# Optimization experiments

Measured on AMD Instinct MI355X. Metric: run time of the kernel, lower is better.

Reference implementation:

```python
import jax, jax.numpy as jnp
import numpy as np

N, T, D, H = 32, 512, 1024, 1024

def setup_inputs() -> dict:
    key = jax.random.key(0)
    k1, k2, k3, k4 = jax.random.split(key, 4)
    x = jax.random.normal(k1, (N, T, D), dtype=jnp.float32)
    prev_ht = jax.random.normal(k2, (N, H), dtype=jnp.float32)
    # scale like a fan-in init so sigmoid/tanh stay in sane range
    weight = jax.random.normal(k3, (D + H, 3 * (D + H)), dtype=jnp.float32) / np.sqrt(D + H)
    bias = jax.random.normal(k4, (3 * (D + H),), dtype=jnp.float32) * 0.01
    return {"x": x, "prev_ht": prev_ht, "weight": weight, "bias": bias}


def reference(x, prev_ht, weight, bias):
    # zoneout = zoneoutd = 0, inference-mode math of GRIDGRUFunction.forward
    Dd = x.shape[2]
    Hh = prev_ht.shape[1]
    Wxt = weight[:Dd, :3 * Hh]            # (D, 3H)
    Wxd = weight[:Dd, 3 * Hh:]            # (D, 3D)
    Whd = weight[Dd:, 3 * Hh:]            # (H, 3D)
    Whtg = weight[Dd:, :2 * Hh]           # (H, 2H)
    Wsmall = weight[Dd:, 2 * Hh:3 * Hh]   # (H, H)
    bt = bias[:3 * Hh]
    bd = bias[3 * Hh:]

    # temporal gate pre-activations from x, computed once: (N, T, 3H)
    gates = jnp.einsum('ntd,dk->ntk', x, Wxt) + bt

    def step(h, g):
        # g: (N, 3H) ; h: (N, H)
        ur = jax.nn.sigmoid(g[:, :2 * Hh] + h @ Whtg)
        u = ur[:, :Hh]
        r = ur[:, Hh:]
        hc = jnp.tanh(g[:, 2 * Hh:] + (r * h) @ Wsmall)
        h_next = h + u * (hc - h)
        return h_next, h_next

    last_h, ht = jax.lax.scan(step, prev_ht, jnp.swapaxes(gates, 0, 1))
    ht = jnp.swapaxes(ht, 0, 1)  # (N, T, H)

    # depth GRU (applied at every (n, t) position)
    urd = jax.nn.sigmoid(bd[:2 * Dd]
                         + jnp.einsum('ntd,dk->ntk', x, Wxd[:, :2 * Dd])
                         + jnp.einsum('nth,hk->ntk', ht, Whd[:, :2 * Dd]))
    ud = urd[..., :Dd]
    rd = urd[..., Dd:]
    hcd = jnp.tanh(bd[2 * Dd:]
                   + jnp.einsum('nth,hk->ntk', ht, Whd[:, 2 * Dd:])
                   + jnp.einsum('ntd,dk->ntk', rd * x, Wxd[:, 2 * Dd:]))
    h = x + ud * (hcd - x)
    return h, last_h
```

## Files before the change

kernel.cpp:

```cpp
#include <hip/hip_runtime.h>
#include <cmath>


#define LDW 6144
#define CT 32
typedef float  f32x4 __attribute__((ext_vector_type(4)));
typedef short  s16x8 __attribute__((ext_vector_type(8)));
typedef unsigned u32x4 __attribute__((ext_vector_type(4)));

__device__ __forceinline__ float sigf(float v){ return 1.f/(1.f+__expf(-v)); }
__device__ __forceinline__ unsigned short f2b(float f){
    unsigned u = __float_as_uint(f);
    return (unsigned short)((u + 0x7FFFu + ((u>>16)&1u)) >> 16);
}
__device__ __forceinline__ float b2f(unsigned short u){
    return __uint_as_float(((unsigned)u) << 16);
}

__device__ __forceinline__ void st_dev_u32x4(unsigned* p, u32x4 v){
    asm volatile("global_store_dwordx4 %0, %1, off sc1"
                 :: "v"(p), "v"(v) : "memory");
}
__device__ __forceinline__ void st_dev_u32(unsigned* p, unsigned v){
    asm volatile("global_store_dword %0, %1, off sc1"
                 :: "v"(p), "v"(v) : "memory");
}
__device__ __forceinline__ unsigned ld_dev_u32(const unsigned* p){
    unsigned v;
    asm volatile("global_load_dword %0, %1, off sc1\n\t"
                 "s_waitcnt vmcnt(0)"
                 : "=v"(v) : "v"(p) : "memory");
    return v;
}

__global__ __launch_bounds__(256)
void k_wt(const float* __restrict__ w, unsigned short* __restrict__ wt)
{
    __shared__ float t[64][65];
    const int j0 = blockIdx.x*64, k0 = blockIdx.y*64;
    for (int i = threadIdx.x; i < 4096; i += 256) {
        int r = i>>6, c = i&63;
        t[r][c] = w[(size_t)(k0+r)*LDW + j0 + c];
    }
    __syncthreads();
    for (int i = threadIdx.x; i < 4096; i += 256) {
        int jr = i>>6, kc = i&63;
        wt[(size_t)(j0+jr)*2048 + k0 + kc] = f2b(t[kc][jr]);
    }
}

__global__ __launch_bounds__(256)
void k_wlo(const float* __restrict__ w, unsigned short* __restrict__ wlo)
{
    __shared__ float t[64][65];
    const int j0 = blockIdx.x*64, k0 = blockIdx.y*64;
    for (int i = threadIdx.x; i < 4096; i += 256) {
        int r = i>>6, c = i&63;
        t[r][c] = w[(size_t)(1024+k0+r)*LDW + j0 + c];
    }
    __syncthreads();
    for (int i = threadIdx.x; i < 4096; i += 256) {
        int jr = i>>6, kc = i&63;
        float v = t[kc][jr];
        unsigned short hi = f2b(v);
        wlo[(size_t)(j0+jr)*1024 + k0 + kc] = f2b(v - b2f(hi));
    }
}

__global__ __launch_bounds__(256)
void k_xbf(const float* __restrict__ x, unsigned short* __restrict__ o)
{
    long i = ((long)blockIdx.x*256 + threadIdx.x)*4;
    float4 v = *(const float4*)&x[i];
    ushort4 r = { f2b(v.x), f2b(v.y), f2b(v.z), f2b(v.w) };
    *(ushort4*)&o[i] = r;
}

template<int AMODE, int EMODE>
__global__ __launch_bounds__(256)
void gemm_mfma(const unsigned short* __restrict__ A1,
               const unsigned short* __restrict__ A2,
               const unsigned short* __restrict__ Bw,
               float* __restrict__ C, int ldc,
               const float* __restrict__ bias,
               const float* __restrict__ X,
               float* __restrict__ UD,
               unsigned short* __restrict__ RX,
               int K, int t0)
{
    __shared__ unsigned short Als[128*32];
    __shared__ unsigned short Bls[128*32];
    const int tid = threadIdx.x;
    const int m_base = blockIdx.y*128;
    const int n_base = blockIdx.x*128;
    const int row0 = tid>>2, row1 = row0+64, quad = tid&3;
    const int wv = tid>>6, lane = tid&63;
    const int wr = (wv>>1)*64, wc = (wv&1)*64;
    const int l15 = lane&15, l4 = lane>>4;

    f32x4 acc[4][4] = {};

    for (int k0 = 0; k0 < K; k0 += 32) {
        const int kq = k0 + quad*8;
        s16x8 a0, a1, b0, b1;
        {
            long r0 = m_base + row0, r1 = m_base + row1;
            const unsigned short *p0, *p1;
            if (AMODE == 1) {
                long g0 = (r0>>5)*512 + t0 + (r0&31);
                long g1 = (r1>>5)*512 + t0 + (r1&31);
                p0 = A1 + g0*1024 + kq; p1 = A1 + g1*1024 + kq;
            } else if (AMODE == 2 && k0 >= 1024) {
                size_t o0 = ((size_t)(r0 & 511)*32 + (r0 >> 9))*1024 + (kq-1024);
                size_t o1 = ((size_t)(r1 & 511)*32 + (r1 >> 9))*1024 + (kq-1024);
                p0 = A2 + o0; p1 = A2 + o1;
            } else {
                p0 = A1 + r0*1024 + kq; p1 = A1 + r1*1024 + kq;
            }
            a0 = *(const s16x8*)p0; a1 = *(const s16x8*)p1;
        }
        b0 = *(const s16x8*)(Bw + (size_t)(n_base+row0)*2048 + kq);
        b1 = *(const s16x8*)(Bw + (size_t)(n_base+row1)*2048 + kq);
        __syncthreads();
        *(s16x8*)&Als[row0*32 + quad*8] = a0;
        *(s16x8*)&Als[row1*32 + quad*8] = a1;
        *(s16x8*)&Bls[row0*32 + quad*8] = b0;
        *(s16x8*)&Bls[row1*32 + quad*8] = b1;
        __syncthreads();
        s16x8 af[4], bfr[4];
#pragma unroll
        for (int i = 0; i < 4; ++i) {
            af[i]  = *(const s16x8*)&Als[(wr + i*16 + l15)*32 + l4*8];
            bfr[i] = *(const s16x8*)&Bls[(wc + i*16 + l15)*32 + l4*8];
        }
#pragma unroll
        for (int mi = 0; mi < 4; ++mi)
#pragma unroll
            for (int ni = 0; ni < 4; ++ni)
                acc[mi][ni] = __builtin_amdgcn_mfma_f32_16x16x32_bf16(
                    af[mi], bfr[ni], acc[mi][ni], 0, 0, 0);
    }

#pragma unroll
    for (int mi = 0; mi < 4; ++mi)
#pragma unroll
    for (int ni = 0; ni < 4; ++ni)
#pragma unroll
    for (int q = 0; q < 4; ++q) {
        int row = m_base + wr + mi*16 + l4*4 + q;
        int col = n_base + wc + ni*16 + l15;
        float v = acc[mi][ni][q] + bias[col];
        if (EMODE == 0) {
            C[(size_t)row*ldc + col] = v;
        } else if (EMODE == 1) {
            float s = sigf(v);
            if (col < 1024) {
                UD[(size_t)row*1024 + col] = s;
            } else {
                int jj = col - 1024;
                RX[(size_t)row*1024 + jj] = f2b(s * X[(size_t)row*1024 + jj]);
            }
        } else {
            float hc = tanhf(v);
            float xv = X[(size_t)row*1024 + col];
            float ud = UD[(size_t)row*1024 + col];
            C[(size_t)row*1024 + col] = xv + ud*(hc - xv);
        }
    }
}

__global__ __launch_bounds__(512)
void scan_mfma4(const float* __restrict__ chunk,
                const unsigned short* __restrict__ WT,
                const unsigned short* __restrict__ Wlo,
                const float* __restrict__ prev_ht,
                unsigned* __restrict__ hX,
                unsigned* __restrict__ rhX,
                unsigned short* __restrict__ htR,
                float* __restrict__ hper,
                unsigned* __restrict__ flags,
                int t0, int bidx0)
{
    __shared__ unsigned short shi[16*1032];
    __shared__ unsigned short slo[16*1032];
    __shared__ float hf32[1024];
    __shared__ float uls [1024];
    const int tid = threadIdx.x;
    const int b   = blockIdx.x;
    const int p   = b & 7, g = b >> 3;
    const int w   = tid >> 6;
    const int lane= tid & 63;
    const int l15 = lane & 15, l4 = lane >> 4;
    const int cb  = p * 128;
    const int nsb = g * 8;
    unsigned bidx = (unsigned)bidx0;

    for (int i = tid; i < 8*1032; i += 512) { shi[8*1032 + i] = 0; slo[8*1032 + i] = 0; }
    for (int i = tid; i < 1024; i += 512) {
        int nl = i >> 7, jl = i & 127;
        hf32[i] = (t0 == 0) ? prev_ht[(size_t)(nsb+nl)*1024 + cb + jl]
                            : hper[(size_t)b*1024 + i];
    }

    for (int tl = 0; tl < CT; ++tl) {
        const int t = t0 + tl;

        if (t == 0) {
#pragma unroll 2
            for (int it = 0; it < 4; ++it) {
                int idx = tid + it*512;
                int nl = idx >> 8, k4 = (idx & 255) * 4;
                f32x4 v = *(const f32x4*)&prev_ht[(size_t)(nsb+nl)*1024 + k4];
#pragma unroll
                for (int e = 0; e < 4; ++e) {
                    unsigned short hi = f2b(v[e]);
                    shi[nl*1032 + k4 + e] = hi;
                    slo[nl*1032 + k4 + e] = f2b(v[e] - b2f(hi));
                }
            }
        } else {
            int slot = (tl == 0) ? (CT-1) : (tl-1);
            const unsigned* src = hX + ((size_t)slot*4 + g)*8192;
#pragma unroll 2
            for (int it = 0; it < 4; ++it) {
                int idx = tid + it*512;
                u32x4 v = *(const u32x4*)&src[idx*4];
                int k = idx >> 1, n0 = (idx & 1) * 4;
#pragma unroll
                for (int e = 0; e < 4; ++e) {
                    shi[(n0+e)*1032 + k] = (unsigned short)(v[e] >> 16);
                    slo[(n0+e)*1032 + k] = (unsigned short)(v[e] & 0xffffu);
                }
            }
        }
        __syncthreads();

        {
            f32x4 accU = {0,0,0,0}, accR = {0,0,0,0};
            const unsigned short* bhU = WT  + (size_t)(cb + w*16 + l15)*2048 + 1024 + l4*8;
            const unsigned short* blU = Wlo + (size_t)(cb + w*16 + l15)*1024 + l4*8;
            const unsigned short* bhR = WT  + (size_t)(1024 + cb + w*16 + l15)*2048 + 1024 + l4*8;
            const unsigned short* blR = Wlo + (size_t)(1024 + cb + w*16 + l15)*1024 + l4*8;
            for (int kq = 0; kq < 32; ++kq) {
                const int ka = kq*32 + l4*8;
                s16x8 ah = *(const s16x8*)&shi[l15*1032 + ka];
                s16x8 al = *(const s16x8*)&slo[l15*1032 + ka];
                s16x8 buh = *(const s16x8*)(bhU + kq*32);
                s16x8 bul = *(const s16x8*)(blU + kq*32);
                s16x8 brh = *(const s16x8*)(bhR + kq*32);
                s16x8 brl = *(const s16x8*)(blR + kq*32);
                accU = __builtin_amdgcn_mfma_f32_16x16x32_bf16(ah, buh, accU, 0,0,0);
                accU = __builtin_amdgcn_mfma_f32_16x16x32_bf16(al, buh, accU, 0,0,0);
                accU = __builtin_amdgcn_mfma_f32_16x16x32_bf16(ah, bul, accU, 0,0,0);
                accR = __builtin_amdgcn_mfma_f32_16x16x32_bf16(ah, brh, accR, 0,0,0);
                accR = __builtin_amdgcn_mfma_f32_16x16x32_bf16(al, brh, accR, 0,0,0);
                accR = __builtin_amdgcn_mfma_f32_16x16x32_bf16(ah, brl, accR, 0,0,0);
            }
            if (l4 < 2) {
                const int jl = w*16 + l15;
                const int k  = cb + jl;
                u32x4 pk;
#pragma unroll
                for (int q = 0; q < 4; ++q) {
                    int nl = l4*4 + q;
                    size_t crow = (size_t)(((nsb+nl)<<5) + tl)*3072;
                    float vu = accU[q] + chunk[crow + cb + jl];
                    uls[nl*128 + jl] = sigf(vu);
                    float vr = accR[q] + chunk[crow + 1024 + k];
                    float s  = sigf(vr);
                    float hv = b2f(shi[nl*1032 + k]) + b2f(slo[nl*1032 + k]);
                    float rh = s * hv;
                    unsigned short hi = f2b(rh);
                    unsigned short lo = f2b(rh - b2f(hi));
                    pk[q] = ((unsigned)hi << 16) | lo;
                }
                st_dev_u32x4(&rhX[(((size_t)tl*4 + g)*1024 + k)*8 + l4*4], pk);
            }
        }
        __syncthreads(); ++bidx;
        if (tid == 0) st_dev_u32(&flags[(unsigned)b*32], bidx);
        if (tid < 8) {
            const unsigned* f = &flags[(unsigned)(g*8 + tid)*32];
            while (ld_dev_u32(f) < bidx) __builtin_amdgcn_s_sleep(1);
        }
        __syncthreads();

        {
            const unsigned* src = rhX + ((size_t)tl*4 + g)*8192;
#pragma unroll 2
            for (int it = 0; it < 4; ++it) {
                int idx = tid + it*512;
                u32x4 v = *(const u32x4*)&src[idx*4];
                int k = idx >> 1, n0 = (idx & 1) * 4;
#pragma unroll
                for (int e = 0; e < 4; ++e) {
                    shi[(n0+e)*1032 + k] = (unsigned short)(v[e] >> 16);
                    slo[(n0+e)*1032 + k] = (unsigned short)(v[e] & 0xffffu);
                }
            }
        }
        __syncthreads();

        {
            f32x4 accC = {0,0,0,0};
            const unsigned short* bhC = WT  + (size_t)(2048 + cb + w*16 + l15)*2048 + 1024 + l4*8;
            const unsigned short* blC = Wlo + (size_t)(2048 + cb + w*16 + l15)*1024 + l4*8;
            for (int kq = 0; kq < 32; ++kq) {
                const int ka = kq*32 + l4*8;
                s16x8 ah = *(const s16x8*)&shi[l15*1032 + ka];
                s16x8 al = *(const s16x8*)&slo[l15*1032 + ka];
                s16x8 bh = *(const s16x8*)(bhC + kq*32);
                s16x8 bl = *(const s16x8*)(blC + kq*32);
                accC = __builtin_amdgcn_mfma_f32_16x16x32_bf16(ah, bh, accC, 0,0,0);
                accC = __builtin_amdgcn_mfma_f32_16x16x32_bf16(al, bh, accC, 0,0,0);
                accC = __builtin_amdgcn_mfma_f32_16x16x32_bf16(ah, bl, accC, 0,0,0);
            }
            if (l4 < 2) {
                const int jl = w*16 + l15;
                u32x4 pk;
#pragma unroll
                for (int q = 0; q < 4; ++q) {
                    int nl = l4*4 + q;
                    size_t crow = (size_t)(((nsb+nl)<<5) + tl)*3072;
                    float v = accC[q] + chunk[crow + 2048 + cb + jl];
                    float hcv  = tanhf(v);
                    float hold = hf32[nl*128 + jl];
                    float uu   = uls [nl*128 + jl];
                    float hn = hold + uu*(hcv - hold);
                    hf32[nl*128 + jl] = hn;
                    unsigned short hi = f2b(hn);
                    unsigned short lo = f2b(hn - b2f(hi));
                    pk[q] = ((unsigned)hi << 16) | lo;
                    htR[((size_t)t*32 + (nsb+nl))*1024 + cb + jl] = hi;
                    if (tl == CT-1) hper[(size_t)b*1024 + nl*128 + jl] = hn;
                }
                st_dev_u32x4(&hX[(((size_t)tl*4 + g)*1024 + (cb+jl))*8 + l4*4], pk);
            }
        }
        __syncthreads(); ++bidx;
        if (tid == 0) st_dev_u32(&flags[(unsigned)b*32], bidx);
        if (tid < 8) {
            const unsigned* f = &flags[(unsigned)(g*8 + tid)*32];
            while (ld_dev_u32(f) < bidx) __builtin_amdgcn_s_sleep(1);
        }
        __syncthreads();
    }
}

__global__ __launch_bounds__(256)
void k_lasth(const float* __restrict__ hper, float* __restrict__ dst)
{
    int i = blockIdx.x*256 + threadIdx.x;
    int n = i >> 10, j = i & 1023;
    dst[i] = hper[(((size_t)(n >> 3)*8 + (j >> 7)))*1024 + (n & 7)*128 + (j & 127)];
}

extern "C" void kernel_launch(void* const* d_in, const int* in_sizes, int n_in,
                              void* d_out, int out_size, void* d_ws, size_t ws_size,
                              hipStream_t stream)
{
    const float* x       = (const float*)d_in[0];
    const float* prev_ht = (const float*)d_in[1];
    const float* weight  = (const float*)d_in[2];
    const float* bias    = (const float*)d_in[3];
    float* out = (float*)d_out;
    float* ws  = (float*)d_ws;

    unsigned short* WT   = (unsigned short*)ws;
    unsigned short* Wlo  = (unsigned short*)(ws + 6291456);
    unsigned short* htR  = (unsigned short*)(ws + 7864320);
    unsigned short* xbf  = (unsigned short*)(ws + 16252928);
    float* zone          = ws + 24641536;
    float* chunk         = zone;
    unsigned* hX         = (unsigned*)(zone + 3145728);
    unsigned* rhX        = (unsigned*)(zone + 4194304);
    unsigned short* rxbf = (unsigned short*)zone;
    float* hper          = ws + 33030144;
    unsigned* flags      = (unsigned*)(ws + 33062912);
    const size_t needed = (size_t)33071104 * 4;
    if (ws_size < needed) return;

    hipMemsetAsync(flags, 0, 4096, stream);
    k_wt <<<dim3(96,32), 256, 0, stream>>>(weight, WT);
    k_wlo<<<dim3(48,16), 256, 0, stream>>>(weight, Wlo);
    k_xbf<<<16384, 256, 0, stream>>>(x, xbf);

    for (int seg = 0; seg < 16; ++seg) {
        int t0 = seg * CT;
        int bidx0 = seg * (2*CT);
        gemm_mfma<1,0><<<dim3(24,8), 256, 0, stream>>>(
            xbf, nullptr, WT, chunk, 3072, bias, nullptr, nullptr, nullptr,
            1024, t0);
        const float* gc = chunk;
        const unsigned short* WTc = WT;
        const unsigned short* Wloc = Wlo;
        void* args[] = { (void*)&gc, (void*)&WTc, (void*)&Wloc, (void*)&prev_ht,
                         (void*)&hX, (void*)&rhX, (void*)&htR, (void*)&hper,
                         (void*)&flags, (void*)&t0, (void*)&bidx0 };
        hipLaunchCooperativeKernel((void*)scan_mfma4, dim3(32), dim3(512),
                                   args, 0, stream);
    }

    gemm_mfma<2,1><<<dim3(16,128), 256, 0, stream>>>(
        xbf, htR, WT + (size_t)3072*2048, nullptr, 0, bias + 3072,
        x, out, rxbf, 2048, 0);
    gemm_mfma<2,2><<<dim3(8,128), 256, 0, stream>>>(
        rxbf, htR, WT + (size_t)5120*2048, out, 1024, bias + 5120,
        x, out, nullptr, 2048, 0);

    k_lasth<<<128, 256, 0, stream>>>(hper, out + (size_t)16384*1024);
}
```

Before: 23.88 ms.

## Assign scan slots by XCD and pack hi/lo recurrent weights per column group

```diff
diff --git a/kernel.cpp b/kernel.cpp
--- a/kernel.cpp
+++ b/kernel.cpp
@@ -21,16 +21,9 @@
     asm volatile("global_store_dwordx4 %0, %1, off sc1"
                  :: "v"(p), "v"(v) : "memory");
 }
-__device__ __forceinline__ void st_dev_u32(unsigned* p, unsigned v){
-    asm volatile("global_store_dword %0, %1, off sc1"
-                 :: "v"(p), "v"(v) : "memory");
-}
-__device__ __forceinline__ unsigned ld_dev_u32(const unsigned* p){
-    unsigned v;
-    asm volatile("global_load_dword %0, %1, off sc1\n\t"
-                 "s_waitcnt vmcnt(0)"
-                 : "=v"(v) : "v"(p) : "memory");
-    return v;
+__device__ __forceinline__ unsigned a_add(unsigned* p, unsigned v){
+    return __hip_atomic_fetch_add(p, v, __ATOMIC_RELAXED,
+                                  __HIP_MEMORY_SCOPE_AGENT);
 }
 
 __global__ __launch_bounds__(256)
@@ -50,7 +43,7 @@
 }
 
 __global__ __launch_bounds__(256)
-void k_wlo(const float* __restrict__ w, unsigned short* __restrict__ wlo)
+void k_wpack(const float* __restrict__ w, unsigned short* __restrict__ wpk)
 {
     __shared__ float t[64][65];
     const int j0 = blockIdx.x*64, k0 = blockIdx.y*64;
@@ -61,9 +54,14 @@
     __syncthreads();
     for (int i = threadIdx.x; i < 4096; i += 256) {
         int jr = i>>6, kc = i&63;
+        int j = j0 + jr, k = k0 + kc;
         float v = t[kc][jr];
         unsigned short hi = f2b(v);
-        wlo[(size_t)(j0+jr)*1024 + k0 + kc] = f2b(v - b2f(hi));
+        unsigned short lo = f2b(v - b2f(hi));
+        int gi = j >> 10, rem = j & 1023, p = rem >> 7, c = rem & 127;
+        size_t base = (size_t)p*786432 + (size_t)gi*262144 + (size_t)c*2048;
+        wpk[base + k]        = hi;
+        wpk[base + 1024 + k] = lo;
     }
 }
 
@@ -170,36 +168,65 @@
 }
 
 __global__ __launch_bounds__(512)
-void scan_mfma4(const float* __restrict__ chunk,
-                const unsigned short* __restrict__ WT,
-                const unsigned short* __restrict__ Wlo,
+void scan_mfma6(const float* __restrict__ chunk,
+                const unsigned short* __restrict__ Wpk,
                 const float* __restrict__ prev_ht,
                 unsigned* __restrict__ hX,
                 unsigned* __restrict__ rhX,
                 unsigned short* __restrict__ htR,
                 float* __restrict__ hper,
                 unsigned* __restrict__ flags,
-                int t0, int bidx0)
+                unsigned* __restrict__ abar,
+                unsigned* __restrict__ xcnt,
+                int t0, int bidx0, unsigned abar_target)
 {
     __shared__ unsigned short shi[16*1032];
     __shared__ unsigned short slo[16*1032];
     __shared__ float hf32[1024];
     __shared__ float uls [1024];
+    __shared__ int   sh_slot;
+    __shared__ unsigned sh_fpos;
     const int tid = threadIdx.x;
-    const int b   = blockIdx.x;
-    const int p   = b & 7, g = b >> 3;
     const int w   = tid >> 6;
     const int lane= tid & 63;
     const int l15 = lane & 15, l4 = lane >> 4;
+    unsigned bidx = (unsigned)bidx0;
+
+    if (tid == 0) {
+        unsigned xcd;
+        asm volatile("s_getreg_b32 %0, hwreg(HW_REG_XCC_ID)" : "=s"(xcd));
+        xcd &= 7u;
+        unsigned pos = a_add(&xcnt[xcd], 1u);
+        int slot = (pos < 4u) ? (int)(xcd*4u + pos) : -1;
+        unsigned fpos = 0u;
+        if (slot < 0) fpos = a_add(&xcnt[8], 1u);
+        sh_slot = slot; sh_fpos = fpos;
+        a_add(abar, 1u);
+        while (a_add(abar, 0u) < abar_target) __builtin_amdgcn_s_sleep(1);
+        if (sh_slot < 0) {
+            unsigned want = sh_fpos, k = 0; int s2 = -1;
+            for (int p2 = 0; p2 < 8 && s2 < 0; ++p2) {
+                unsigned c = a_add(&xcnt[p2], 0u);
+                if (c > 4u) c = 4u;
+                for (unsigned g2 = c; g2 < 4u && s2 < 0; ++g2, ++k)
+                    if (k == want) s2 = p2*4 + (int)g2;
+            }
+            sh_slot = s2;
+        }
+    }
+    __syncthreads();
+    const int slot = sh_slot;
+    const int p = slot >> 2, g = slot & 3;
     const int cb  = p * 128;
     const int nsb = g * 8;
-    unsigned bidx = (unsigned)bidx0;
+    unsigned* ownf = &flags[(unsigned)slot*32];
+    const unsigned short* wbase = Wpk + (size_t)p*786432;
 
     for (int i = tid; i < 8*1032; i += 512) { shi[8*1032 + i] = 0; slo[8*1032 + i] = 0; }
     for (int i = tid; i < 1024; i += 512) {
         int nl = i >> 7, jl = i & 127;
         hf32[i] = (t0 == 0) ? prev_ht[(size_t)(nsb+nl)*1024 + cb + jl]
-                            : hper[(size_t)b*1024 + i];
+                            : hper[(size_t)slot*1024 + i];
     }
 
     for (int tl = 0; tl < CT; ++tl) {
@@ -219,8 +246,8 @@
                 }
             }
         } else {
-            int slot = (tl == 0) ? (CT-1) : (tl-1);
-            const unsigned* src = hX + ((size_t)slot*4 + g)*8192;
+            int slotr = (tl == 0) ? (CT-1) : (tl-1);
+            const unsigned* src = hX + ((size_t)slotr*4 + g)*8192;
 #pragma unroll 2
             for (int it = 0; it < 4; ++it) {
                 int idx = tid + it*512;
@@ -237,18 +264,16 @@
 
         {
             f32x4 accU = {0,0,0,0}, accR = {0,0,0,0};
-            const unsigned short* bhU = WT  + (size_t)(cb + w*16 + l15)*2048 + 1024 + l4*8;
-            const unsigned short* blU = Wlo + (size_t)(cb + w*16 + l15)*1024 + l4*8;
-            const unsigned short* bhR = WT  + (size_t)(1024 + cb + w*16 + l15)*2048 + 1024 + l4*8;
-            const unsigned short* blR = Wlo + (size_t)(1024 + cb + w*16 + l15)*1024 + l4*8;
+            const unsigned short* bhU = wbase +          (size_t)(w*16 + l15)*2048 + l4*8;
+            const unsigned short* bhR = wbase + 262144 + (size_t)(w*16 + l15)*2048 + l4*8;
             for (int kq = 0; kq < 32; ++kq) {
                 const int ka = kq*32 + l4*8;
                 s16x8 ah = *(const s16x8*)&shi[l15*1032 + ka];
                 s16x8 al = *(const s16x8*)&slo[l15*1032 + ka];
                 s16x8 buh = *(const s16x8*)(bhU + kq*32);
-                s16x8 bul = *(const s16x8*)(blU + kq*32);
+                s16x8 bul = *(const s16x8*)(bhU + 1024 + kq*32);
                 s16x8 brh = *(const s16x8*)(bhR + kq*32);
-                s16x8 brl = *(const s16x8*)(blR + kq*32);
+                s16x8 brl = *(const s16x8*)(bhR + 1024 + kq*32);
                 accU = __builtin_amdgcn_mfma_f32_16x16x32_bf16(ah, buh, accU, 0,0,0);
                 accU = __builtin_amdgcn_mfma_f32_16x16x32_bf16(al, buh, accU, 0,0,0);
                 accU = __builtin_amdgcn_mfma_f32_16x16x32_bf16(ah, bul, accU, 0,0,0);
@@ -277,11 +302,12 @@
                 st_dev_u32x4(&rhX[(((size_t)tl*4 + g)*1024 + k)*8 + l4*4], pk);
             }
         }
+        asm volatile("s_waitcnt vmcnt(0)" ::: "memory");
         __syncthreads(); ++bidx;
-        if (tid == 0) st_dev_u32(&flags[(unsigned)b*32], bidx);
+        if (tid == 0) a_add(ownf, 1u);
         if (tid < 8) {
-            const unsigned* f = &flags[(unsigned)(g*8 + tid)*32];
-            while (ld_dev_u32(f) < bidx) __builtin_amdgcn_s_sleep(1);
+            unsigned* f = &flags[(unsigned)(tid*4 + g)*32];
+            while (a_add(f, 0u) < bidx) __builtin_amdgcn_s_sleep(1);
         }
         __syncthreads();
 
@@ -303,14 +329,13 @@
 
         {
             f32x4 accC = {0,0,0,0};
-            const unsigned short* bhC = WT  + (size_t)(2048 + cb + w*16 + l15)*2048 + 1024 + l4*8;
-            const unsigned short* blC = Wlo + (size_t)(2048 + cb + w*16 + l15)*1024 + l4*8;
+            const unsigned short* bhC = wbase + 524288 + (size_t)(w*16 + l15)*2048 + l4*8;
             for (int kq = 0; kq < 32; ++kq) {
                 const int ka = kq*32 + l4*8;
                 s16x8 ah = *(const s16x8*)&shi[l15*1032 + ka];
                 s16x8 al = *(const s16x8*)&slo[l15*1032 + ka];
                 s16x8 bh = *(const s16x8*)(bhC + kq*32);
-                s16x8 bl = *(const s16x8*)(blC + kq*32);
+                s16x8 bl = *(const s16x8*)(bhC + 1024 + kq*32);
                 accC = __builtin_amdgcn_mfma_f32_16x16x32_bf16(ah, bh, accC, 0,0,0);
                 accC = __builtin_amdgcn_mfma_f32_16x16x32_bf16(al, bh, accC, 0,0,0);
                 accC = __builtin_amdgcn_mfma_f32_16x16x32_bf16(ah, bl, accC, 0,0,0);
@@ -332,19 +357,25 @@
                     unsigned short lo = f2b(hn - b2f(hi));
                     pk[q] = ((unsigned)hi << 16) | lo;
                     htR[((size_t)t*32 + (nsb+nl))*1024 + cb + jl] = hi;
-                    if (tl == CT-1) hper[(size_t)b*1024 + nl*128 + jl] = hn;
+                    if (tl == CT-1) hper[(size_t)slot*1024 + nl*128 + jl] = hn;
                 }
                 st_dev_u32x4(&hX[(((size_t)tl*4 + g)*1024 + (cb+jl))*8 + l4*4], pk);
             }
         }
+        asm volatile("s_waitcnt vmcnt(0)" ::: "memory");
         __syncthreads(); ++bidx;
-        if (tid == 0) st_dev_u32(&flags[(unsigned)b*32], bidx);
+        if (tid == 0) a_add(ownf, 1u);
         if (tid < 8) {
-            const unsigned* f = &flags[(unsigned)(g*8 + tid)*32];
-            while (ld_dev_u32(f) < bidx) __builtin_amdgcn_s_sleep(1);
-        }
-        __syncthreads();
-    }
+            unsigned* f = &flags[(unsigned)(tid*4 + g)*32];
+            while (a_add(f, 0u) < bidx) __builtin_amdgcn_s_sleep(1);
+        }
+        __syncthreads();
+    }
+
+    if (slot == 0 && tid == 0)
+        for (int i = 0; i < 9; ++i)
+            __hip_atomic_store(&xcnt[i], 0u, __ATOMIC_RELAXED,
+                               __HIP_MEMORY_SCOPE_AGENT);
 }
 
 __global__ __launch_bounds__(256)
@@ -352,7 +383,8 @@
 {
     int i = blockIdx.x*256 + threadIdx.x;
     int n = i >> 10, j = i & 1023;
-    dst[i] = hper[(((size_t)(n >> 3)*8 + (j >> 7)))*1024 + (n & 7)*128 + (j & 127)];
+    int p = j >> 7, jl = j & 127, g = n >> 3, nl = n & 7;
+    dst[i] = hper[((size_t)(p*4 + g))*1024 + nl*128 + jl];
 }
 
 extern "C" void kernel_launch(void* const* d_in, const int* in_sizes, int n_in,
@@ -367,37 +399,40 @@
     float* ws  = (float*)d_ws;
 
     unsigned short* WT   = (unsigned short*)ws;
-    unsigned short* Wlo  = (unsigned short*)(ws + 6291456);
-    unsigned short* htR  = (unsigned short*)(ws + 7864320);
-    unsigned short* xbf  = (unsigned short*)(ws + 16252928);
-    float* zone          = ws + 24641536;
+    unsigned short* htR  = (unsigned short*)(ws + 6291456);
+    unsigned short* xbf  = (unsigned short*)(ws + 14680064);
+    float* zone          = ws + 23068672;
     float* chunk         = zone;
     unsigned* hX         = (unsigned*)(zone + 3145728);
     unsigned* rhX        = (unsigned*)(zone + 4194304);
+    unsigned short* Wpk  = (unsigned short*)(zone + 5242880);
     unsigned short* rxbf = (unsigned short*)zone;
-    float* hper          = ws + 33030144;
-    unsigned* flags      = (unsigned*)(ws + 33062912);
-    const size_t needed = (size_t)33071104 * 4;
+    float* hper          = ws + 31457280;
+    unsigned* flags      = (unsigned*)(ws + 31490048);
+    unsigned* abar       = flags + 1024;
+    unsigned* xcnt       = flags + 1056;
+    const size_t needed = (size_t)31498240 * 4;
     if (ws_size < needed) return;
 
-    hipMemsetAsync(flags, 0, 4096, stream);
-    k_wt <<<dim3(96,32), 256, 0, stream>>>(weight, WT);
-    k_wlo<<<dim3(48,16), 256, 0, stream>>>(weight, Wlo);
-    k_xbf<<<16384, 256, 0, stream>>>(x, xbf);
+    hipMemsetAsync(flags, 0, 32768, stream);
+    k_wt   <<<dim3(96,32), 256, 0, stream>>>(weight, WT);
+    k_wpack<<<dim3(48,16), 256, 0, stream>>>(weight, Wpk);
+    k_xbf  <<<16384, 256, 0, stream>>>(x, xbf);
 
     for (int seg = 0; seg < 16; ++seg) {
         int t0 = seg * CT;
         int bidx0 = seg * (2*CT);
+        unsigned abar_target = 32u * (unsigned)(seg + 1);
         gemm_mfma<1,0><<<dim3(24,8), 256, 0, stream>>>(
             xbf, nullptr, WT, chunk, 3072, bias, nullptr, nullptr, nullptr,
             1024, t0);
         const float* gc = chunk;
-        const unsigned short* WTc = WT;
-        const unsigned short* Wloc = Wlo;
-        void* args[] = { (void*)&gc, (void*)&WTc, (void*)&Wloc, (void*)&prev_ht,
+        const unsigned short* Wpkc = Wpk;
+        void* args[] = { (void*)&gc, (void*)&Wpkc, (void*)&prev_ht,
                          (void*)&hX, (void*)&rhX, (void*)&htR, (void*)&hper,
-                         (void*)&flags, (void*)&t0, (void*)&bidx0 };
-        hipLaunchCooperativeKernel((void*)scan_mfma4, dim3(32), dim3(512),
+                         (void*)&flags, (void*)&abar, (void*)&xcnt,
+                         (void*)&t0, (void*)&bidx0, (void*)&abar_target };
+        hipLaunchCooperativeKernel((void*)scan_mfma6, dim3(32), dim3(512),
                                    args, 0, stream);
     }
 
```

New measurement: 23.94 ms. About the same (+0.3%).
